# Optimization experiments

Hardware: AMD Instinct MI355X
Metric: run time of the kernel (lower is better)

The kernel has to match this reference:

```python
import jax, jax.numpy as jnp
import numpy as np

N_NODES = 50000
N_EDGES = 800000
IN_FEATS = 128
OUT_FEATS = 128


def setup_inputs() -> dict:
    key = jax.random.key(0)
    k1, k2, k3, k4 = jax.random.split(key, 4)
    feature = jax.random.normal(k1, (N_NODES, IN_FEATS), dtype=jnp.float32)
    src = jax.random.randint(k2, (N_EDGES,), 0, N_NODES, dtype=jnp.int64)
    dst = jax.random.randint(k3, (N_EDGES,), 0, N_NODES, dtype=jnp.int64)
    # nn.Linear(in_feats, out_feats): W is [out, in], b is [out]
    bound = 1.0 / np.sqrt(IN_FEATS)
    W = jax.random.uniform(k4, (OUT_FEATS, IN_FEATS), minval=-bound, maxval=bound, dtype=jnp.float32)
    b = jnp.zeros((OUT_FEATS,), dtype=jnp.float32)
    return {"feature": feature, "src": src, "dst": dst, "W": W, "b": b}


def reference(feature, src, dst, W, b):
    # DGL update_all(copy_src('h'), sum('m','h')): h'[v] = sum over edges u->v of h[u]
    n_nodes = feature.shape[0]
    msgs = feature[src]  # [E, in_feats] gather
    agg = jax.ops.segment_sum(msgs, dst, num_segments=n_nodes)  # [N, in_feats]
    # linear: agg @ W.T + b
    return jnp.einsum("ni,oi->no", agg, W) + b
```

## Files before the change

### kernel.cpp

```cpp
#include <hip/hip_runtime.h>
#include <hip/hip_bf16.h>

#define N_FEATS 128
#define SCAN_CHUNK 1024

__global__ void gcn_init(const float* __restrict__ W, float* __restrict__ Wt,
                         int* __restrict__ deg, int n_nodes) {
    int t = blockIdx.x * blockDim.x + threadIdx.x;
    if (t < N_FEATS * N_FEATS) {
        int o = t >> 7;
        int i = t & 127;
        Wt[i * N_FEATS + o] = W[o * N_FEATS + i];
    }
    int u = t - N_FEATS * N_FEATS;
    if (u >= 0 && u < n_nodes) deg[u] = 0;
}

__global__ void gcn_hist_pos(const int* __restrict__ src, const int* __restrict__ dst,
                             int* __restrict__ deg, int* __restrict__ pos,
                             int n_edges, int n_nodes) {
    int e = blockIdx.x * blockDim.x + threadIdx.x;
    if (e >= n_edges) return;
    int d = dst[e];
    int s = src[e];
    if ((unsigned)d < (unsigned)n_nodes && (unsigned)s < (unsigned)n_nodes)
        pos[e] = atomicAdd(&deg[d], 1);
}

__global__ void gcn_hist(const int* __restrict__ src, const int* __restrict__ dst,
                         int* __restrict__ deg, int n_edges, int n_nodes) {
    int e = blockIdx.x * blockDim.x + threadIdx.x;
    if (e >= n_edges) return;
    int d = dst[e];
    int s = src[e];
    if ((unsigned)d < (unsigned)n_nodes && (unsigned)s < (unsigned)n_nodes)
        atomicAdd(&deg[d], 1);
}

__launch_bounds__(256)
__global__ void gcn_scan_part(const int* __restrict__ deg, int* __restrict__ chunk_sum, int n) {
    const int t = threadIdx.x;
    const int base = blockIdx.x * SCAN_CHUNK;
    int sum = 0;
#pragma unroll
    for (int k = 0; k < 4; ++k) {
        int idx = base + k * 256 + t;
        if (idx < n) sum += deg[idx];
    }
    for (int d = 1; d < 64; d <<= 1) sum += __shfl_xor(sum, d, 64);
    __shared__ int wsum[4];
    if ((t & 63) == 0) wsum[t >> 6] = sum;
    __syncthreads();
    if (t == 0) chunk_sum[blockIdx.x] = wsum[0] + wsum[1] + wsum[2] + wsum[3];
}

__launch_bounds__(256)
__global__ void gcn_scan_final(const int* __restrict__ deg, const int* __restrict__ chunk_sum,
                               int* __restrict__ row_start, int* __restrict__ cursor,
                               int n, int nchunks) {
    const int t = threadIdx.x;
    const int b = blockIdx.x;

    int v = 0;
    for (int j = t; j < b; j += 256) v += chunk_sum[j];
    for (int d = 1; d < 64; d <<= 1) v += __shfl_xor(v, d, 64);
    __shared__ int owsum[4];
    __shared__ int s_off;
    if ((t & 63) == 0) owsum[t >> 6] = v;
    __syncthreads();
    if (t == 0) s_off = owsum[0] + owsum[1] + owsum[2] + owsum[3];
    __syncthreads();
    const int chunk_off = s_off;

    const int base = b * SCAN_CHUNK;
    const int idx0 = base + t * 4;
    int x[4];
#pragma unroll
    for (int k = 0; k < 4; ++k) {
        int idx = idx0 + k;
        x[k] = (idx < n) ? deg[idx] : 0;
    }
    const int tsum = x[0] + x[1] + x[2] + x[3];

    const int lane = t & 63, w = t >> 6;
    int inc = tsum;
    for (int d = 1; d < 64; d <<= 1) {
        int sv = __shfl_up(inc, d, 64);
        if (lane >= d) inc += sv;
    }
    __shared__ int wsum[4];
    if (lane == 63) wsum[w] = inc;
    __syncthreads();
    int woff = 0;
    for (int i = 0; i < w; ++i) woff += wsum[i];

    int run = chunk_off + woff + inc - tsum;
#pragma unroll
    for (int k = 0; k < 4; ++k) {
        int idx = idx0 + k;
        if (idx < n) {
            row_start[idx] = run;
            if (cursor) cursor[idx] = 0;
        }
        run += x[k];
    }

    if (t == 0 && b == nchunks - 1)
        row_start[n] = chunk_off + wsum[0] + wsum[1] + wsum[2] + wsum[3];
}

__global__ void gcn_build_csr_pos(const int* __restrict__ src, const int* __restrict__ dst,
                                  const int* __restrict__ row_start, const int* __restrict__ pos,
                                  int* __restrict__ csr_src, int n_edges, int n_nodes) {
    int e = blockIdx.x * blockDim.x + threadIdx.x;
    if (e >= n_edges) return;
    int d = dst[e];
    int s = src[e];
    if ((unsigned)d >= (unsigned)n_nodes || (unsigned)s >= (unsigned)n_nodes) return;
    csr_src[row_start[d] + pos[e]] = s;
}

__global__ void gcn_build_csr(const int* __restrict__ src, const int* __restrict__ dst,
                              const int* __restrict__ row_start, int* __restrict__ cursor,
                              int* __restrict__ csr_src, int n_edges, int n_nodes) {
    int e = blockIdx.x * blockDim.x + threadIdx.x;
    if (e >= n_edges) return;
    int d = dst[e];
    int s = src[e];
    if ((unsigned)d >= (unsigned)n_nodes || (unsigned)s >= (unsigned)n_nodes) return;
    int p = atomicAdd(&cursor[d], 1);
    csr_src[row_start[d] + p] = s;
}

__launch_bounds__(256)
__global__ void gcn_aggregate(const float* __restrict__ feat,
                              const int* __restrict__ row_start,
                              const int* __restrict__ csr_src,
                              float* __restrict__ out, int n_nodes) {
    int node = blockIdx.x * 4 + (threadIdx.x >> 6);
    if (node >= n_nodes) return;
    const int l = threadIdx.x & 63;
    const int q = l & 31;
    const int h = l >> 5;
    int beg = row_start[node];
    int end = row_start[node + 1];
    const float4* f4 = reinterpret_cast<const float4*>(feat);

    float4 a0 = make_float4(0.f, 0.f, 0.f, 0.f);
    float4 a1 = a0, a2 = a0, a3 = a0;
    int i = beg;
    for (; i + 8 <= end; i += 8) {
        int s0 = csr_src[i + h];
        int s1 = csr_src[i + 2 + h];
        int s2 = csr_src[i + 4 + h];
        int s3 = csr_src[i + 6 + h];
        float4 v0 = f4[(size_t)s0 * 32 + q];
        float4 v1 = f4[(size_t)s1 * 32 + q];
        float4 v2 = f4[(size_t)s2 * 32 + q];
        float4 v3 = f4[(size_t)s3 * 32 + q];
        a0.x += v0.x; a0.y += v0.y; a0.z += v0.z; a0.w += v0.w;
        a1.x += v1.x; a1.y += v1.y; a1.z += v1.z; a1.w += v1.w;
        a2.x += v2.x; a2.y += v2.y; a2.z += v2.z; a2.w += v2.w;
        a3.x += v3.x; a3.y += v3.y; a3.z += v3.z; a3.w += v3.w;
    }
    for (; i + 2 <= end; i += 2) {
        int s0 = csr_src[i + h];
        float4 v0 = f4[(size_t)s0 * 32 + q];
        a0.x += v0.x; a0.y += v0.y; a0.z += v0.z; a0.w += v0.w;
    }
    if (i < end && h == 0) {
        int s = csr_src[i];
        float4 v = f4[(size_t)s * 32 + q];
        a0.x += v.x; a0.y += v.y; a0.z += v.z; a0.w += v.w;
    }

    float4 acc = make_float4(a0.x + a1.x + a2.x + a3.x,
                             a0.y + a1.y + a2.y + a3.y,
                             a0.z + a1.z + a2.z + a3.z,
                             a0.w + a1.w + a2.w + a3.w);
    acc.x += __shfl_xor(acc.x, 32, 64);
    acc.y += __shfl_xor(acc.y, 32, 64);
    acc.z += __shfl_xor(acc.z, 32, 64);
    acc.w += __shfl_xor(acc.w, 32, 64);

    if (h == 0)
        reinterpret_cast<float4*>(out)[(size_t)node * 32 + q] = acc;
}

__global__ void gcn_scatter_add(const float* __restrict__ feat,
                                const int* __restrict__ src,
                                const int* __restrict__ dst,
                                float* __restrict__ agg,
                                int n_edges, int n_nodes) {
    long long tid = (long long)blockIdx.x * blockDim.x + threadIdx.x;
    int e = (int)(tid >> 5);
    if (e >= n_edges) return;
    int j = (int)(tid & 31);
    int s = src[e];
    int d = dst[e];
    if ((unsigned)s >= (unsigned)n_nodes || (unsigned)d >= (unsigned)n_nodes) return;
    const float4 v = *reinterpret_cast<const float4*>(feat + (size_t)s * N_FEATS + j * 4);
    float* p = agg + (size_t)d * N_FEATS + j * 4;
    atomicAdd(p + 0, v.x);
    atomicAdd(p + 1, v.y);
    atomicAdd(p + 2, v.z);
    atomicAdd(p + 3, v.w);
}

__launch_bounds__(256)
__global__ void gcn_gemm_inplace(float* __restrict__ out,
                                 const float* __restrict__ Wt,
                                 const float* __restrict__ b,
                                 int n_nodes) {
    __shared__ float a_lds[32 * N_FEATS];

    const int t = threadIdx.x;
    const int node0 = blockIdx.x * 32;
    const int rows = min(32, n_nodes - node0);

    float4* a4 = reinterpret_cast<float4*>(a_lds);
    const float4* out4 = reinterpret_cast<const float4*>(out + (size_t)node0 * N_FEATS);
    const int nflt4 = rows * (N_FEATS / 4);
    for (int idx = t; idx < nflt4; idx += 256) a4[idx] = out4[idx];
    __syncthreads();

    const int oq = t & 31;
    const int ng = t >> 5;

    const float4 bb = reinterpret_cast<const float4*>(b)[oq];
    float4 acc[4];
#pragma unroll
    for (int k = 0; k < 4; ++k) acc[k] = bb;

    const float4* Wt4 = reinterpret_cast<const float4*>(Wt);
#pragma unroll 4
    for (int i = 0; i < N_FEATS; ++i) {
        const float4 w = Wt4[i * 32 + oq];
#pragma unroll
        for (int k = 0; k < 4; ++k) {
            const float a = a_lds[(ng * 4 + k) * N_FEATS + i];
            acc[k].x += a * w.x;
            acc[k].y += a * w.y;
            acc[k].z += a * w.z;
            acc[k].w += a * w.w;
        }
    }

    __syncthreads();

#pragma unroll
    for (int k = 0; k < 4; ++k) {
        const int r = ng * 4 + k;
        if (r < rows) {
            reinterpret_cast<float4*>(out + (size_t)(node0 + r) * N_FEATS)[oq] = acc[k];
        }
    }
}

extern "C" void kernel_launch(void* const* d_in, const int* in_sizes, int n_in,
                              void* d_out, int out_size, void* d_ws, size_t ws_size,
                              hipStream_t stream) {
    const float* feature = (const float*)d_in[0];
    const int*   src     = (const int*)d_in[1];
    const int*   dst     = (const int*)d_in[2];
    const float* W       = (const float*)d_in[3];
    const float* b       = (const float*)d_in[4];
    float* out = (float*)d_out;

    const int n_nodes = in_sizes[0] / N_FEATS;
    const int n_edges = in_sizes[1];
    const int nchunks = (n_nodes + SCAN_CHUNK - 1) / SCAN_CHUNK;

    char* ws = (char*)d_ws;
    size_t off = 0;
    auto take = [&](size_t bytes) -> char* {
        char* p = ws + off;
        off = (off + bytes + 255) & ~(size_t)255;
        return p;
    };
    float* Wt        = (float*)take((size_t)N_FEATS * N_FEATS * sizeof(float));
    int*   deg       = (int*)  take((size_t)n_nodes * sizeof(int));
    int*   row_start = (int*)  take(((size_t)n_nodes + 1) * sizeof(int));
    int*   chunk_sum = (int*)  take((size_t)nchunks * sizeof(int));
    int*   csr_src   = (int*)  take((size_t)n_edges * sizeof(int));
    const size_t off_common = off;
    int* pos    = (int*)take((size_t)n_edges * sizeof(int));
    const bool tierA = (off <= ws_size);
    off = off_common;
    int* cursor = (int*)take((size_t)n_nodes * sizeof(int));
    const bool tierB = !tierA && (off <= ws_size);

    if (tierA || tierB) {
        int init_elems = N_FEATS * N_FEATS + n_nodes;
        gcn_init<<<(init_elems + 255) / 256, 256, 0, stream>>>(W, Wt, deg, n_nodes);
        const int eblocks = (n_edges + 255) / 256;
        if (tierA) {
            gcn_hist_pos<<<eblocks, 256, 0, stream>>>(src, dst, deg, pos, n_edges, n_nodes);
        } else {
            gcn_hist<<<eblocks, 256, 0, stream>>>(src, dst, deg, n_edges, n_nodes);
        }
        gcn_scan_part<<<nchunks, 256, 0, stream>>>(deg, chunk_sum, n_nodes);
        gcn_scan_final<<<nchunks, 256, 0, stream>>>(deg, chunk_sum, row_start,
                                                    tierA ? (int*)nullptr : cursor,
                                                    n_nodes, nchunks);
        if (tierA) {
            gcn_build_csr_pos<<<eblocks, 256, 0, stream>>>(
                src, dst, row_start, pos, csr_src, n_edges, n_nodes);
        } else {
            gcn_build_csr<<<eblocks, 256, 0, stream>>>(
                src, dst, row_start, cursor, csr_src, n_edges, n_nodes);
        }
        gcn_aggregate<<<(n_nodes + 3) / 4, 256, 0, stream>>>(
            feature, row_start, csr_src, out, n_nodes);
    } else {
        gcn_init<<<(N_FEATS * N_FEATS + 255) / 256, 256, 0, stream>>>(W, Wt, deg, 0);
        hipMemsetAsync(d_out, 0, (size_t)n_nodes * N_FEATS * sizeof(float), stream);
        long long total = (long long)n_edges * 32;
        gcn_scatter_add<<<(int)((total + 255) / 256), 256, 0, stream>>>(
            feature, src, dst, out, n_edges, n_nodes);
    }

    gcn_gemm_inplace<<<(n_nodes + 31) / 32, 256, 0, stream>>>(out, Wt, b, n_nodes);
}
```

Before: 150.7 us.

## Gather bf16 copy of node features during CSR aggregation

Adds a cast of the feature matrix to bf16 inside the init kernel and a new aggregation kernel that gathers bf16 rows, with 16 lanes per row and four edges in flight per wavefront, accumulating in fp32. This halves the bytes moved by the random-access gather, which dominates the aggregation. In exchange it adds a full pass that reads and writes the feature matrix, plus extra workspace, and it lowers input precision, which may push results past tolerance.

```diff
diff --git a/kernel.cpp b/kernel.cpp
--- a/kernel.cpp
+++ b/kernel.cpp
@@ -4,15 +4,35 @@
 #define N_FEATS 128
 #define SCAN_CHUNK 1024
 
+__device__ __forceinline__ unsigned short f32_to_bf16_rne(float f) {
+    unsigned u = __float_as_uint(f);
+    u = u + 0x7FFFu + ((u >> 16) & 1u);
+    return (unsigned short)(u >> 16);
+}
+
 __global__ void gcn_init(const float* __restrict__ W, float* __restrict__ Wt,
-                         int* __restrict__ deg, int n_nodes) {
+                         const float* __restrict__ feat, unsigned short* __restrict__ featb,
+                         int cast_chunks, int* __restrict__ deg, int n_nodes) {
     int t = blockIdx.x * blockDim.x + threadIdx.x;
-    if (t < N_FEATS * N_FEATS) {
-        int o = t >> 7;
-        int i = t & 127;
+    if (t < cast_chunks) {
+        const float4* f4 = reinterpret_cast<const float4*>(feat) + (size_t)t * 2;
+        float4 x0 = f4[0];
+        float4 x1 = f4[1];
+        ushort4 o0, o1;
+        o0.x = f32_to_bf16_rne(x0.x); o0.y = f32_to_bf16_rne(x0.y);
+        o0.z = f32_to_bf16_rne(x0.z); o0.w = f32_to_bf16_rne(x0.w);
+        o1.x = f32_to_bf16_rne(x1.x); o1.y = f32_to_bf16_rne(x1.y);
+        o1.z = f32_to_bf16_rne(x1.z); o1.w = f32_to_bf16_rne(x1.w);
+        reinterpret_cast<ushort4*>(featb)[(size_t)t * 2 + 0] = o0;
+        reinterpret_cast<ushort4*>(featb)[(size_t)t * 2 + 1] = o1;
+    }
+    int t2 = t - cast_chunks;
+    if (t2 >= 0 && t2 < N_FEATS * N_FEATS) {
+        int o = t2 >> 7;
+        int i = t2 & 127;
         Wt[i * N_FEATS + o] = W[o * N_FEATS + i];
     }
-    int u = t - N_FEATS * N_FEATS;
+    int u = t2 - N_FEATS * N_FEATS;
     if (u >= 0 && u < n_nodes) deg[u] = 0;
 }
 
@@ -130,6 +150,83 @@
     if ((unsigned)d >= (unsigned)n_nodes || (unsigned)s >= (unsigned)n_nodes) return;
     int p = atomicAdd(&cursor[d], 1);
     csr_src[row_start[d] + p] = s;
+}
+
+#define BACC(acc, v)                                              \
+    do {                                                          \
+        unsigned uu;                                              \
+        uu = (v).x;                                               \
+        acc[0] += __uint_as_float(uu << 16);                      \
+        acc[1] += __uint_as_float(uu & 0xFFFF0000u);              \
+        uu = (v).y;                                               \
+        acc[2] += __uint_as_float(uu << 16);                      \
+        acc[3] += __uint_as_float(uu & 0xFFFF0000u);              \
+        uu = (v).z;                                               \
+        acc[4] += __uint_as_float(uu << 16);                      \
+        acc[5] += __uint_as_float(uu & 0xFFFF0000u);              \
+        uu = (v).w;                                               \
+        acc[6] += __uint_as_float(uu << 16);                      \
+        acc[7] += __uint_as_float(uu & 0xFFFF0000u);              \
+    } while (0)
+
+__launch_bounds__(256)
+__global__ void gcn_aggregate_bf16(const uint4* __restrict__ featb,
+                                   const int* __restrict__ row_start,
+                                   const int* __restrict__ csr_src,
+                                   float* __restrict__ out, int n_nodes) {
+    int node = blockIdx.x * 4 + (threadIdx.x >> 6);
+    if (node >= n_nodes) return;
+    const int l = threadIdx.x & 63;
+    const int qw = l >> 4;
+    const int ql = l & 15;
+    int beg = row_start[node];
+    int end = row_start[node + 1];
+
+    float a0[8] = {0,0,0,0,0,0,0,0};
+    float a1[8] = {0,0,0,0,0,0,0,0};
+    float a2[8] = {0,0,0,0,0,0,0,0};
+    float a3[8] = {0,0,0,0,0,0,0,0};
+
+    int i = beg;
+    for (; i + 16 <= end; i += 16) {
+        int s0 = csr_src[i + qw];
+        int s1 = csr_src[i + 4 + qw];
+        int s2 = csr_src[i + 8 + qw];
+        int s3 = csr_src[i + 12 + qw];
+        uint4 v0 = featb[(size_t)s0 * 16 + ql];
+        uint4 v1 = featb[(size_t)s1 * 16 + ql];
+        uint4 v2 = featb[(size_t)s2 * 16 + ql];
+        uint4 v3 = featb[(size_t)s3 * 16 + ql];
+        BACC(a0, v0);
+        BACC(a1, v1);
+        BACC(a2, v2);
+        BACC(a3, v3);
+    }
+    for (; i + 4 <= end; i += 4) {
+        int s = csr_src[i + qw];
+        uint4 v = featb[(size_t)s * 16 + ql];
+        BACC(a0, v);
+    }
+    int rem = end - i;
+    if (qw < rem) {
+        int s = csr_src[i + qw];
+        uint4 v = featb[(size_t)s * 16 + ql];
+        BACC(a0, v);
+    }
+
+    float r[8];
+#pragma unroll
+    for (int k = 0; k < 8; ++k) {
+        r[k] = a0[k] + a1[k] + a2[k] + a3[k];
+        r[k] += __shfl_xor(r[k], 16, 64);
+        r[k] += __shfl_xor(r[k], 32, 64);
+    }
+
+    if (qw == 0) {
+        float4* o4 = reinterpret_cast<float4*>(out + (size_t)node * N_FEATS + ql * 8);
+        o4[0] = make_float4(r[0], r[1], r[2], r[3]);
+        o4[1] = make_float4(r[4], r[5], r[6], r[7]);
+    }
 }
 
 __launch_bounds__(256)
@@ -284,36 +381,51 @@
     int*   chunk_sum = (int*)  take((size_t)nchunks * sizeof(int));
     int*   csr_src   = (int*)  take((size_t)n_edges * sizeof(int));
     const size_t off_common = off;
-    int* pos    = (int*)take((size_t)n_edges * sizeof(int));
-    const bool tierA = (off <= ws_size);
+
+    unsigned short* featb = (unsigned short*)take((size_t)n_nodes * N_FEATS * sizeof(unsigned short));
+    int* posA2 = (int*)take((size_t)n_edges * sizeof(int));
+    const bool tierA2 = (off <= ws_size);
+    off = off_common;
+    int* posA = (int*)take((size_t)n_edges * sizeof(int));
+    const bool tierA = !tierA2 && (off <= ws_size);
     off = off_common;
     int* cursor = (int*)take((size_t)n_nodes * sizeof(int));
-    const bool tierB = !tierA && (off <= ws_size);
-
-    if (tierA || tierB) {
-        int init_elems = N_FEATS * N_FEATS + n_nodes;
-        gcn_init<<<(init_elems + 255) / 256, 256, 0, stream>>>(W, Wt, deg, n_nodes);
+    const bool tierB = !tierA2 && !tierA && (off <= ws_size);
+
+    if (tierA2 || tierA || tierB) {
+        const int cast_chunks = tierA2 ? (n_nodes * (N_FEATS / 8)) : 0;
+        const int init_elems = cast_chunks + N_FEATS * N_FEATS + n_nodes;
+        gcn_init<<<(init_elems + 255) / 256, 256, 0, stream>>>(
+            W, Wt, feature, featb, cast_chunks, deg, n_nodes);
+
         const int eblocks = (n_edges + 255) / 256;
-        if (tierA) {
+        int* pos = tierA2 ? posA2 : posA;
+        if (tierA2 || tierA) {
             gcn_hist_pos<<<eblocks, 256, 0, stream>>>(src, dst, deg, pos, n_edges, n_nodes);
         } else {
             gcn_hist<<<eblocks, 256, 0, stream>>>(src, dst, deg, n_edges, n_nodes);
         }
         gcn_scan_part<<<nchunks, 256, 0, stream>>>(deg, chunk_sum, n_nodes);
         gcn_scan_final<<<nchunks, 256, 0, stream>>>(deg, chunk_sum, row_start,
-                                                    tierA ? (int*)nullptr : cursor,
+                                                    (tierA2 || tierA) ? (int*)nullptr : cursor,
                                                     n_nodes, nchunks);
-        if (tierA) {
+        if (tierA2 || tierA) {
             gcn_build_csr_pos<<<eblocks, 256, 0, stream>>>(
                 src, dst, row_start, pos, csr_src, n_edges, n_nodes);
         } else {
             gcn_build_csr<<<eblocks, 256, 0, stream>>>(
                 src, dst, row_start, cursor, csr_src, n_edges, n_nodes);
         }
-        gcn_aggregate<<<(n_nodes + 3) / 4, 256, 0, stream>>>(
-            feature, row_start, csr_src, out, n_nodes);
+        if (tierA2) {
+            gcn_aggregate_bf16<<<(n_nodes + 3) / 4, 256, 0, stream>>>(
+                reinterpret_cast<const uint4*>(featb), row_start, csr_src, out, n_nodes);
+        } else {
+            gcn_aggregate<<<(n_nodes + 3) / 4, 256, 0, stream>>>(
+                feature, row_start, csr_src, out, n_nodes);
+        }
     } else {
-        gcn_init<<<(N_FEATS * N_FEATS + 255) / 256, 256, 0, stream>>>(W, Wt, deg, 0);
+        gcn_init<<<(N_FEATS * N_FEATS + 255) / 256, 256, 0, stream>>>(
+            W, Wt, feature, (unsigned short*)nullptr, 0, deg, 0);
         hipMemsetAsync(d_out, 0, (size_t)n_nodes * N_FEATS * sizeof(float), stream);
         long long total = (long long)n_edges * 32;
         gcn_scatter_add<<<(int)((total + 255) / 256), 256, 0, stream>>>(
```

After: 133.4 us. -11.4%, faster.
